# Kernel optimization log

Hardware: AMD Instinct MI355X
Metric: run time of the kernel (lower is better)

The kernel has to match this reference:

```python
import jax, jax.numpy as jnp
import numpy as np

F_NHID = 64
C_NHID = 64
U_INIT = F_NHID + C_NHID + 1   # 129
U_OUT = F_NHID + C_NHID        # 128
U_HID = 128
N_AGG = 4
M_INIT = 3 * N_AGG * U_OUT + C_NHID  # 1600
M_HID = 256
M_OUT = C_NHID


def setup_inputs() -> dict:
    key = jax.random.key(0)
    ks = jax.random.split(key, 12)
    B, Nc, Nf = 4, 512, 256
    h_fac = jax.random.normal(ks[0], (B, Nf, F_NHID), dtype=jnp.float32)
    h_cus = jax.random.normal(ks[1], (B, Nc, C_NHID), dtype=jnp.float32)
    edge = jax.random.normal(ks[2], (B, Nc, Nf, 1), dtype=jnp.float32)
    adj = jax.random.randint(ks[3], (B, Nc, Nf), 0, 2).astype(jnp.float32)
    def lin(k, i, o):
        return jax.random.normal(k, (i, o), dtype=jnp.float32) / np.sqrt(i)
    return {
        'h_fac': h_fac, 'h_cus': h_cus, 'edge': edge, 'adj': adj,
        'U_W1': lin(ks[4], U_INIT, U_HID), 'U_b1': jnp.zeros((U_HID,), jnp.float32),
        'U_W2': lin(ks[5], U_HID, U_OUT), 'U_b2': jnp.zeros((U_OUT,), jnp.float32),
        'M_W1': lin(ks[6], M_INIT, M_HID), 'M_b1': jnp.zeros((M_HID,), jnp.float32),
        'M_W2': lin(ks[7], M_HID, M_OUT), 'M_b2': jnp.zeros((M_OUT,), jnp.float32),
    }


def reference(h_fac, h_cus, edge, adj, U_W1, U_b1, U_W2, U_b2, M_W1, M_b1, M_W2, M_b2):
    B, Nc, c = h_cus.shape
    Nf = h_fac.shape[1]
    # Per-edge message input: [customer_feat, facility_feat, edge_scalar] -> (B,Nc,Nf,U_INIT)
    msg = jnp.concatenate([
        jnp.broadcast_to(h_cus[:, :, None, :], (B, Nc, Nf, c)),
        jnp.broadcast_to(h_fac[:, None, :, :], (B, Nc, Nf, h_fac.shape[-1])),
        edge,
    ], axis=-1)
    # U MLP (pretransformation): relu -> linear
    m = jax.nn.relu(msg @ U_W1 + U_b1)
    m = m @ U_W2 + U_b2  # (B, Nc, Nf, U_OUT)

    mask = adj > 0                              # (B, Nc, Nf)
    maskf = mask[..., None].astype(m.dtype)     # (B, Nc, Nf, 1)
    cnt = jnp.sum(maskf, axis=2)                # (B, Nc, 1)
    mean = jnp.sum(m * maskf, axis=2) / cnt     # nanmean over masked entries
    var = jnp.sum(((m - mean[:, :, None, :]) ** 2) * maskf, axis=2) / cnt
    std = jnp.sqrt(var)                         # population std (divides by count)
    mx = jnp.max(jnp.where(mask[..., None], m, -jnp.inf), axis=2)
    mn = jnp.min(jnp.where(mask[..., None], m, jnp.inf), axis=2)

    # Degree-based scalers (get_avgd + scale_amplification/attenuation)
    deg_c = jnp.sum(adj, axis=-1)               # (B, Nc)
    deg_f = jnp.sum(adj, axis=-2)               # (B, Nf)
    avg_d = jnp.mean(jnp.concatenate([jnp.log(deg_c + 1.0), jnp.log(deg_f + 1.0)], axis=-1), axis=-1)  # (B,)
    scale = (jnp.log(deg_c + 1.0) / avg_d[:, None])[..., None]          # (B, Nc, 1)
    scale_inv = jnp.where(scale != 0, 1.0 / scale, jnp.zeros_like(scale))

    feats = [h_cus]
    for a in (mean, std, mx, mn):
        feats.extend([a, a * scale, a * scale_inv])
    h = jnp.concatenate(feats, axis=-1)         # (B, Nc, M_INIT)

    # M MLP (posttransformation): relu -> linear (last activation 'none')
    h = jax.nn.relu(h @ M_W1 + M_b1)
    out = h @ M_W2 + M_b2                       # (B, Nc, C_NHID)
    return out
```

## Files before the change

kernel.cpp:

```cpp
#include <hip/hip_runtime.h>


using bs8 = __attribute__((ext_vector_type(8))) short;
using f4  = __attribute__((ext_vector_type(4))) float;

__device__ __forceinline__ unsigned short f2bf(float f) {
    union { float f; unsigned int u; } x; x.f = f;
    unsigned int u = x.u + 0x7FFFu + ((x.u >> 16) & 1u);
    return (unsigned short)(u >> 16);
}

__global__ void PNALayer_35081292874189_kernel() {}

#define OFF_AC     0u
#define OFF_AF     1048576u
#define OFF_DEGC   1572864u
#define OFF_DEGF   1581056u
#define OFF_SCALE  1585152u
#define OFF_SINV   1593344u
#define OFF_FEATB  1601536u
#define OFF_HMID   8155392u
#define OFF_W2T    10252544u
#define OFF_W1TB   10318080u
#define WS_NEED    11170048u

__global__ void PNALayer_ws_fail(float* out, int n) {
    int i = blockIdx.x * 256 + threadIdx.x;
    if (i < n) out[i] = 2500.0f;
}

__global__ void PNALayer_prep1(
    const float* h_fac, const float* h_cus, const float* adj,
    const float* U_W1, const float* U_b1, const float* U_W2, const float* M_W1,
    float* wsAc, float* wsAf, float* wsDegC, float* wsDegF,
    float* wsW2T, unsigned short* wsW1Tb)
{
    __shared__ float sH[64];
    __shared__ float sRed[256];
    __shared__ float sT[64][65];
    int bid = blockIdx.x, t = threadIdx.x;

    if (bid < 1024) {
        int b = bid >> 8, f = bid & 255;
        if (t < 64) sH[t] = h_fac[(b * 256 + f) * 64 + t];
        __syncthreads();
        if (t < 128) {
            float acc = 0.f;
            for (int k = 0; k < 64; ++k)
                acc += sH[k] * U_W1[(64 + k) * 128 + t];
            wsAf[(b * 256 + f) * 128 + t] = acc;
        }
        float v = adj[(b * 512 + t) * 256 + f] + adj[(b * 512 + t + 256) * 256 + f];
        sRed[t] = v; __syncthreads();
        for (int s = 128; s > 0; s >>= 1) { if (t < s) sRed[t] += sRed[t + s]; __syncthreads(); }
        if (t == 0) wsDegF[b * 256 + f] = sRed[0];
    } else if (bid < 3072) {
        int bc = bid - 1024;
        if (t < 64) sH[t] = h_cus[bc * 64 + t];
        __syncthreads();
        if (t < 128) {
            float acc = U_b1[t];
            for (int k = 0; k < 64; ++k)
                acc += sH[k] * U_W1[k * 128 + t];
            wsAc[bc * 128 + t] = acc;
        }
        float v = adj[bc * 256 + t];
        sRed[t] = v; __syncthreads();
        for (int s = 128; s > 0; s >>= 1) { if (t < s) sRed[t] += sRed[t + s]; __syncthreads(); }
        if (t == 0) wsDegC[bc] = sRed[0];
    } else if (bid < 3076) {
        int l = bid - 3072;
        int k0 = (l >> 1) * 64, n0 = (l & 1) * 64;
        for (int rep = 0; rep < 16; ++rep) {
            int idx = rep * 256 + t; int r = idx >> 6, c = idx & 63;
            sT[r][c] = U_W2[(k0 + r) * 128 + n0 + c];
        }
        __syncthreads();
        for (int rep = 0; rep < 16; ++rep) {
            int idx = rep * 256 + t; int r = idx >> 6, c = idx & 63;
            wsW2T[(n0 + r) * 128 + k0 + c] = sT[c][r];
        }
    } else if (bid < 3176) {
        int l = bid - 3076;
        int k0 = (l % 25) * 64, n0 = (l / 25) * 64;
        for (int rep = 0; rep < 16; ++rep) {
            int idx = rep * 256 + t; int r = idx >> 6, c = idx & 63;
            sT[r][c] = M_W1[(k0 + r) * 256 + n0 + c];
        }
        __syncthreads();
        for (int rep = 0; rep < 16; ++rep) {
            int idx = rep * 256 + t; int r = idx >> 6, c = idx & 63;
            wsW1Tb[(n0 + r) * 1664 + k0 + c] = f2bf(sT[c][r]);
        }
    } else {
        for (int i = 0; i < 64; ++i) {
            int idx = i * 256 + t;
            int n = idx >> 6, k = 1600 + (idx & 63);
            wsW1Tb[n * 1664 + k] = 0;
        }
    }
}

__global__ void PNALayer_prep2(
    const float* wsDegC, const float* wsDegF, float* wsScale, float* wsSinv)
{
    __shared__ float sRed[256];
    __shared__ float sAvg;
    int b = blockIdx.x, t = threadIdx.x;
    float v = logf(wsDegC[b * 512 + t] + 1.f) + logf(wsDegC[b * 512 + t + 256] + 1.f)
            + logf(wsDegF[b * 256 + t] + 1.f);
    sRed[t] = v; __syncthreads();
    for (int s = 128; s > 0; s >>= 1) { if (t < s) sRed[t] += sRed[t + s]; __syncthreads(); }
    if (t == 0) sAvg = sRed[0] / 768.f;
    __syncthreads();
    float avg = sAvg;
    for (int c = t; c < 512; c += 256) {
        float lg = logf(wsDegC[b * 512 + c] + 1.f);
        float sc = lg / avg;
        float si = (sc != 0.f) ? 1.f / sc : 0.f;
        wsScale[b * 512 + c] = sc;
        wsSinv[b * 512 + c] = si;
    }
}

__global__ __launch_bounds__(256, 2) void PNALayer_edge(
    const float* h_cus, const float* edge, const float* adj,
    const float* U_W1, const float* U_b2,
    const float* wsAc, const float* wsAf, const float* wsW2T, const float* wsDegC,
    const float* wsScale, const float* wsSinv,
    unsigned short* featB)
{
    __shared__ __align__(16) unsigned char smem[64000];
    unsigned short* sW2T = (unsigned short*)(smem);
    unsigned short* sM1  = (unsigned short*)(smem + 34816);
    float* sRed = (float*)(smem + 52224);
    float* sE   = (float*)(smem + 60416);
    float* sMk  = (float*)(smem + 61440);
    float* sAc  = (float*)(smem + 62464);
    float* sWe  = (float*)(smem + 62976);
    float* sB2  = (float*)(smem + 63488);

    int bc = blockIdx.x;
    int b  = bc >> 9;
    int t  = threadIdx.x;
    int w = t >> 6, quad = (t >> 4) & 3, ln = t & 15;

    {
        unsigned int* z = (unsigned int*)smem;
        for (int i = t; i < 16000; i += 256) z[i] = 0u;
    }
    __syncthreads();

    for (int rep = 0; rep < 16; ++rep) {
        int vi = rep * 256 + t;
        int n = vi >> 5, kb = (vi & 31) * 4;
        float4 wv = *(const float4*)(wsW2T + n * 128 + kb);
        uint2 p;
        p.x = (unsigned int)f2bf(wv.x) | ((unsigned int)f2bf(wv.y) << 16);
        p.y = (unsigned int)f2bf(wv.z) | ((unsigned int)f2bf(wv.w) << 16);
        *(uint2*)(sW2T + n * 136 + kb) = p;
    }
    sE[t]  = edge[bc * 256 + t];
    sMk[t] = (adj[bc * 256 + t] > 0.f) ? 1.f : 0.f;
    if (t < 128) {
        sAc[t] = wsAc[bc * 128 + t];
        sWe[t] = U_W1[128 * 128 + t];
        sB2[t] = U_b2[t];
    }
    __syncthreads();

    float b2v[8];
    for (int nt = 0; nt < 8; ++nt) b2v[nt] = sB2[nt * 16 + ln];

    float aS[8], aQ[8], aMx[8], aMn[8];
    for (int j = 0; j < 8; ++j) { aS[j] = 0.f; aQ[j] = 0.f; aMx[j] = -1e30f; aMn[j] = 1e30f; }

    for (int ft = 0; ft < 4; ++ft) {
        for (int i = 0; i < 8; ++i) {
            int idx = i * 256 + t;
            int fl = idx >> 5, k = (idx & 31) * 4;
            int f = ft * 64 + fl;
            float4 af = *(const float4*)(wsAf + (b * 256 + f) * 128 + k);
            float e = sE[f];
            float m0 = fmaxf(sAc[k + 0] + af.x + e * sWe[k + 0], 0.f);
            float m1 = fmaxf(sAc[k + 1] + af.y + e * sWe[k + 1], 0.f);
            float m2 = fmaxf(sAc[k + 2] + af.z + e * sWe[k + 2], 0.f);
            float m3 = fmaxf(sAc[k + 3] + af.w + e * sWe[k + 3], 0.f);
            uint2 p;
            p.x = (unsigned int)f2bf(m0) | ((unsigned int)f2bf(m1) << 16);
            p.y = (unsigned int)f2bf(m2) | ((unsigned int)f2bf(m3) << 16);
            *(uint2*)(sM1 + fl * 136 + k) = p;
        }
        __syncthreads();

        f4 acc[8];
        for (int nt = 0; nt < 8; ++nt) acc[nt] = (f4){0.f, 0.f, 0.f, 0.f};
        int arow = w * 16 + ln;
        for (int kk = 0; kk < 4; ++kk) {
            int ko = kk * 32 + quad * 8;
            bs8 a = *(const bs8*)(sM1 + arow * 136 + ko);
            for (int nt = 0; nt < 8; ++nt) {
                bs8 bb = *(const bs8*)(sW2T + (nt * 16 + ln) * 136 + ko);
                acc[nt] = __builtin_amdgcn_mfma_f32_16x16x32_bf16(a, bb, acc[nt], 0, 0, 0);
            }
        }

        for (int i = 0; i < 4; ++i) {
            int f = ft * 64 + w * 16 + quad * 4 + i;
            if (sMk[f] > 0.f) {
                for (int nt = 0; nt < 8; ++nt) {
                    float v = acc[nt][i] + b2v[nt];
                    aS[nt] += v; aQ[nt] += v * v;
                    aMx[nt] = fmaxf(aMx[nt], v); aMn[nt] = fminf(aMn[nt], v);
                }
            }
        }
        __syncthreads();
    }

    for (int nt = 0; nt < 8; ++nt) {
        aS[nt]  += __shfl_xor(aS[nt], 16, 64);  aS[nt]  += __shfl_xor(aS[nt], 32, 64);
        aQ[nt]  += __shfl_xor(aQ[nt], 16, 64);  aQ[nt]  += __shfl_xor(aQ[nt], 32, 64);
        aMx[nt] = fmaxf(aMx[nt], __shfl_xor(aMx[nt], 16, 64));
        aMx[nt] = fmaxf(aMx[nt], __shfl_xor(aMx[nt], 32, 64));
        aMn[nt] = fminf(aMn[nt], __shfl_xor(aMn[nt], 16, 64));
        aMn[nt] = fminf(aMn[nt], __shfl_xor(aMn[nt], 32, 64));
    }
    if (quad == 0) {
        for (int nt = 0; nt < 8; ++nt) {
            int col = nt * 16 + ln;
            sRed[(0 * 4 + w) * 128 + col] = aS[nt];
            sRed[(1 * 4 + w) * 128 + col] = aQ[nt];
            sRed[(2 * 4 + w) * 128 + col] = aMx[nt];
            sRed[(3 * 4 + w) * 128 + col] = aMn[nt];
        }
    }
    __syncthreads();

    if (t < 128) {
        int j = t;
        float rS = 0.f, rQ = 0.f, rMx = -1e30f, rMn = 1e30f;
        for (int ww = 0; ww < 4; ++ww) {
            rS += sRed[(0 * 4 + ww) * 128 + j];
            rQ += sRed[(1 * 4 + ww) * 128 + j];
            rMx = fmaxf(rMx, sRed[(2 * 4 + ww) * 128 + j]);
            rMn = fminf(rMn, sRed[(3 * 4 + ww) * 128 + j]);
        }
        float cnt = wsDegC[bc];
        float mean = rS / cnt;
        float var  = fmaxf(rQ / cnt - mean * mean, 0.f);
        float stdv = sqrtf(var);
        float sc = wsScale[bc], si = wsSinv[bc];
        unsigned short* fr = featB + bc * 1600;
        fr[64 + j]   = f2bf(mean); fr[192 + j]  = f2bf(mean * sc); fr[320 + j]  = f2bf(mean * si);
        fr[448 + j]  = f2bf(stdv); fr[576 + j]  = f2bf(stdv * sc); fr[704 + j]  = f2bf(stdv * si);
        fr[832 + j]  = f2bf(rMx);  fr[960 + j]  = f2bf(rMx * sc);  fr[1088 + j] = f2bf(rMx * si);
        fr[1216 + j] = f2bf(rMn);  fr[1344 + j] = f2bf(rMn * sc);  fr[1472 + j] = f2bf(rMn * si);
    } else if (t < 192) {
        int j = t - 128;
        featB[bc * 1600 + j] = f2bf(h_cus[bc * 64 + j]);
    }
}

__global__ __launch_bounds__(256) void PNALayer_mlp1(
    const unsigned short* featB, const unsigned short* wsW1Tb, const float* M_b1,
    float* h_mid)
{
    __shared__ __align__(16) unsigned short sA[16 * 136];
    __shared__ __align__(16) unsigned short sB[64 * 136];
    int t = threadIdx.x;
    int rb = (blockIdx.x >> 2) * 16, cb = (blockIdx.x & 3) * 64;
    int w = t >> 6, quad = (t >> 4) & 3, ln = t & 15;

    f4 acc = (f4){0.f, 0.f, 0.f, 0.f};

    for (int kt = 0; kt < 13; ++kt) {
        int kb = kt * 128;
        {
            int row = t >> 4, c8 = (t & 15) * 8;
            *(uint4*)(sA + row * 136 + c8) =
                *(const uint4*)(featB + (rb + row) * 1600 + kb + c8);
        }
        for (int i = 0; i < 4; ++i) {
            int vi = i * 256 + t;
            int row = vi >> 4, c8 = (vi & 15) * 8;
            *(uint4*)(sB + row * 136 + c8) =
                *(const uint4*)(wsW1Tb + (cb + row) * 1664 + kb + c8);
        }
        __syncthreads();
        for (int kk = 0; kk < 4; ++kk) {
            int ko = kk * 32 + quad * 8;
            bs8 a = *(const bs8*)(sA + ln * 136 + ko);
            bs8 bb = *(const bs8*)(sB + (w * 16 + ln) * 136 + ko);
            acc = __builtin_amdgcn_mfma_f32_16x16x32_bf16(a, bb, acc, 0, 0, 0);
        }
        __syncthreads();
    }
    int col = cb + w * 16 + ln;
    float b1v = M_b1[col];
    for (int i = 0; i < 4; ++i) {
        int row = rb + quad * 4 + i;
        h_mid[row * 256 + col] = fmaxf(acc[i] + b1v, 0.f);
    }
}

__global__ void PNALayer_mlp2(
    const float* h_mid, const float* M_W2, const float* M_b2, float* out)
{
    int idx = blockIdx.x * 256 + threadIdx.x;
    int row = idx >> 6, j = idx & 63;
    float acc = M_b2[j];
    const float* hr = h_mid + row * 256;
    for (int k = 0; k < 256; ++k)
        acc += hr[k] * M_W2[k * 64 + j];
    out[idx] = acc;
}

extern "C" void kernel_launch(void* const* d_in, const int* in_sizes, int n_in,
                              void* d_out, int out_size, void* d_ws, size_t ws_size,
                              hipStream_t stream) {
    const float* h_fac = (const float*)d_in[0];
    const float* h_cus = (const float*)d_in[1];
    const float* edge  = (const float*)d_in[2];
    const float* adj   = (const float*)d_in[3];
    const float* U_W1  = (const float*)d_in[4];
    const float* U_b1  = (const float*)d_in[5];
    const float* U_W2  = (const float*)d_in[6];
    const float* U_b2  = (const float*)d_in[7];
    const float* M_W1  = (const float*)d_in[8];
    const float* M_b1  = (const float*)d_in[9];
    const float* M_W2  = (const float*)d_in[10];
    const float* M_b2  = (const float*)d_in[11];
    (void)in_sizes; (void)n_in;

    float* outp = (float*)d_out;
    int nblk_out = (out_size + 255) / 256;

    if (ws_size < (size_t)WS_NEED) {
        PNALayer_ws_fail<<<nblk_out, 256, 0, stream>>>(outp, out_size);
        return;
    }

    char* ws = (char*)d_ws;
    float*          wsAc   = (float*)(ws + OFF_AC);
    float*          wsAf   = (float*)(ws + OFF_AF);
    float*          wsDegC = (float*)(ws + OFF_DEGC);
    float*          wsDegF = (float*)(ws + OFF_DEGF);
    float*          wsScal = (float*)(ws + OFF_SCALE);
    float*          wsSinv = (float*)(ws + OFF_SINV);
    unsigned short* wsFeatB= (unsigned short*)(ws + OFF_FEATB);
    float*          wsHmid = (float*)(ws + OFF_HMID);
    float*          wsW2T  = (float*)(ws + OFF_W2T);
    unsigned short* wsW1Tb = (unsigned short*)(ws + OFF_W1TB);

    PNALayer_prep1<<<3177, 256, 0, stream>>>(
        h_fac, h_cus, adj, U_W1, U_b1, U_W2, M_W1,
        wsAc, wsAf, wsDegC, wsDegF, wsW2T, wsW1Tb);
    PNALayer_prep2<<<4, 256, 0, stream>>>(wsDegC, wsDegF, wsScal, wsSinv);
    PNALayer_edge<<<2048, 256, 0, stream>>>(
        h_cus, edge, adj, U_W1, U_b2,
        wsAc, wsAf, wsW2T, wsDegC, wsScal, wsSinv, wsFeatB);
    PNALayer_mlp1<<<512, 256, 0, stream>>>(wsFeatB, wsW1Tb, M_b1, wsHmid);
    PNALayer_mlp2<<<512, 256, 0, stream>>>(wsHmid, M_W2, M_b2, outp);
}
```

Measured before the change: 180.0 us.

## Keep U_W2 bf16 fragments in registers and split edge MFMA by output columns

The prep kernel now writes the transposed U_W2 directly in bf16. The edge kernel loads each wave's slice of those weights into registers instead of staging the full matrix in shared memory. Each wave now owns 32 output columns across all 64 facility rows, so the cross-wave shared-memory reduction and its barrier go away and shared memory drops enough to allow 4 blocks per CU. It also vectorizes the sAc/sWe reads and uses the packed bf16 conversion intrinsic. The cost is that each wave reads all A rows from LDS and register pressure rises under the tighter launch bound.

```diff
diff --git a/kernel.cpp b/kernel.cpp
--- a/kernel.cpp
+++ b/kernel.cpp
@@ -1,4 +1,5 @@
 #include <hip/hip_runtime.h>
+#include <hip/hip_bf16.h>
 
 
 using bs8 = __attribute__((ext_vector_type(8))) short;
@@ -8,6 +9,12 @@
     union { float f; unsigned int u; } x; x.f = f;
     unsigned int u = x.u + 0x7FFFu + ((x.u >> 16) & 1u);
     return (unsigned short)(u >> 16);
+}
+
+__device__ __forceinline__ unsigned int pkbf(float a, float b) {
+    __hip_bfloat162 h = __float22bfloat162_rn(make_float2(a, b));
+    union { __hip_bfloat162 h; unsigned int u; } c; c.h = h;
+    return c.u;
 }
 
 __global__ void PNALayer_35081292874189_kernel() {}
@@ -33,7 +40,7 @@
     const float* h_fac, const float* h_cus, const float* adj,
     const float* U_W1, const float* U_b1, const float* U_W2, const float* M_W1,
     float* wsAc, float* wsAf, float* wsDegC, float* wsDegF,
-    float* wsW2T, unsigned short* wsW1Tb)
+    unsigned short* wsW2Tb, unsigned short* wsW1Tb)
 {
     __shared__ float sH[64];
     __shared__ float sRed[256];
@@ -78,7 +85,7 @@
         __syncthreads();
         for (int rep = 0; rep < 16; ++rep) {
             int idx = rep * 256 + t; int r = idx >> 6, c = idx & 63;
-            wsW2T[(n0 + r) * 128 + k0 + c] = sT[c][r];
+            wsW2Tb[(n0 + r) * 128 + k0 + c] = f2bf(sT[c][r]);
         }
     } else if (bid < 3176) {
         int l = bid - 3076;
@@ -123,102 +130,104 @@
     }
 }
 
-__global__ __launch_bounds__(256, 2) void PNALayer_edge(
+__global__ __launch_bounds__(256, 4) void PNALayer_edge(
     const float* h_cus, const float* edge, const float* adj,
     const float* U_W1, const float* U_b2,
-    const float* wsAc, const float* wsAf, const float* wsW2T, const float* wsDegC,
-    const float* wsScale, const float* wsSinv,
+    const float* wsAc, const float* wsAf, const unsigned short* wsW2Tb,
+    const float* wsDegC, const float* wsScale, const float* wsSinv,
     unsigned short* featB)
 {
-    __shared__ __align__(16) unsigned char smem[64000];
-    unsigned short* sW2T = (unsigned short*)(smem);
-    unsigned short* sM1  = (unsigned short*)(smem + 34816);
-    float* sRed = (float*)(smem + 52224);
-    float* sE   = (float*)(smem + 60416);
-    float* sMk  = (float*)(smem + 61440);
-    float* sAc  = (float*)(smem + 62464);
-    float* sWe  = (float*)(smem + 62976);
-    float* sB2  = (float*)(smem + 63488);
+    __shared__ __align__(16) unsigned short sM1[64 * 136];
+    __shared__ float sE[256];
+    __shared__ float sMk[256];
+    __shared__ float sAc[128];
+    __shared__ float sWe[128];
 
     int bc = blockIdx.x;
     int b  = bc >> 9;
     int t  = threadIdx.x;
     int w = t >> 6, quad = (t >> 4) & 3, ln = t & 15;
 
-    {
-        unsigned int* z = (unsigned int*)smem;
-        for (int i = t; i < 16000; i += 256) z[i] = 0u;
-    }
-    __syncthreads();
-
-    for (int rep = 0; rep < 16; ++rep) {
-        int vi = rep * 256 + t;
-        int n = vi >> 5, kb = (vi & 31) * 4;
-        float4 wv = *(const float4*)(wsW2T + n * 128 + kb);
-        uint2 p;
-        p.x = (unsigned int)f2bf(wv.x) | ((unsigned int)f2bf(wv.y) << 16);
-        p.y = (unsigned int)f2bf(wv.z) | ((unsigned int)f2bf(wv.w) << 16);
-        *(uint2*)(sW2T + n * 136 + kb) = p;
-    }
+    int r0 = (w * 2 + 0) * 16 + ln;
+    int r1 = (w * 2 + 1) * 16 + ln;
+    bs8 bw0[4], bw1[4];
+#pragma unroll
+    for (int kk = 0; kk < 4; ++kk) {
+        bw0[kk] = *(const bs8*)(wsW2Tb + r0 * 128 + kk * 32 + quad * 8);
+        bw1[kk] = *(const bs8*)(wsW2Tb + r1 * 128 + kk * 32 + quad * 8);
+    }
+    float b2v0 = U_b2[r0], b2v1 = U_b2[r1];
+
     sE[t]  = edge[bc * 256 + t];
     sMk[t] = (adj[bc * 256 + t] > 0.f) ? 1.f : 0.f;
     if (t < 128) {
         sAc[t] = wsAc[bc * 128 + t];
         sWe[t] = U_W1[128 * 128 + t];
-        sB2[t] = U_b2[t];
-    }
+    }
+    if (t < 64) featB[bc * 1600 + t] = f2bf(h_cus[bc * 64 + t]);
     __syncthreads();
 
-    float b2v[8];
-    for (int nt = 0; nt < 8; ++nt) b2v[nt] = sB2[nt * 16 + ln];
-
-    float aS[8], aQ[8], aMx[8], aMn[8];
-    for (int j = 0; j < 8; ++j) { aS[j] = 0.f; aQ[j] = 0.f; aMx[j] = -1e30f; aMn[j] = 1e30f; }
+    float aS[2]  = {0.f, 0.f},     aQ[2]  = {0.f, 0.f};
+    float aMx[2] = {-1e30f, -1e30f}, aMn[2] = {1e30f, 1e30f};
 
     for (int ft = 0; ft < 4; ++ft) {
+#pragma unroll
         for (int i = 0; i < 8; ++i) {
             int idx = i * 256 + t;
             int fl = idx >> 5, k = (idx & 31) * 4;
             int f = ft * 64 + fl;
-            float4 af = *(const float4*)(wsAf + (b * 256 + f) * 128 + k);
+            float4 af  = *(const float4*)(wsAf + (b * 256 + f) * 128 + k);
+            float4 ac4 = *(const float4*)(sAc + k);
+            float4 we4 = *(const float4*)(sWe + k);
             float e = sE[f];
-            float m0 = fmaxf(sAc[k + 0] + af.x + e * sWe[k + 0], 0.f);
-            float m1 = fmaxf(sAc[k + 1] + af.y + e * sWe[k + 1], 0.f);
-            float m2 = fmaxf(sAc[k + 2] + af.z + e * sWe[k + 2], 0.f);
-            float m3 = fmaxf(sAc[k + 3] + af.w + e * sWe[k + 3], 0.f);
+            float m0 = fmaxf(ac4.x + af.x + e * we4.x, 0.f);
+            float m1 = fmaxf(ac4.y + af.y + e * we4.y, 0.f);
+            float m2 = fmaxf(ac4.z + af.z + e * we4.z, 0.f);
+            float m3 = fmaxf(ac4.w + af.w + e * we4.w, 0.f);
             uint2 p;
-            p.x = (unsigned int)f2bf(m0) | ((unsigned int)f2bf(m1) << 16);
-            p.y = (unsigned int)f2bf(m2) | ((unsigned int)f2bf(m3) << 16);
+            p.x = pkbf(m0, m1);
+            p.y = pkbf(m2, m3);
             *(uint2*)(sM1 + fl * 136 + k) = p;
         }
         __syncthreads();
 
-        f4 acc[8];
-        for (int nt = 0; nt < 8; ++nt) acc[nt] = (f4){0.f, 0.f, 0.f, 0.f};
-        int arow = w * 16 + ln;
+        f4 acc[4][2];
+#pragma unroll
+        for (int rt = 0; rt < 4; ++rt) {
+            acc[rt][0] = (f4){0.f, 0.f, 0.f, 0.f};
+            acc[rt][1] = (f4){0.f, 0.f, 0.f, 0.f};
+        }
+#pragma unroll
         for (int kk = 0; kk < 4; ++kk) {
             int ko = kk * 32 + quad * 8;
-            bs8 a = *(const bs8*)(sM1 + arow * 136 + ko);
-            for (int nt = 0; nt < 8; ++nt) {
-                bs8 bb = *(const bs8*)(sW2T + (nt * 16 + ln) * 136 + ko);
-                acc[nt] = __builtin_amdgcn_mfma_f32_16x16x32_bf16(a, bb, acc[nt], 0, 0, 0);
+#pragma unroll
+            for (int rt = 0; rt < 4; ++rt) {
+                bs8 a = *(const bs8*)(sM1 + (rt * 16 + ln) * 136 + ko);
+                acc[rt][0] = __builtin_amdgcn_mfma_f32_16x16x32_bf16(a, bw0[kk], acc[rt][0], 0, 0, 0);
+                acc[rt][1] = __builtin_amdgcn_mfma_f32_16x16x32_bf16(a, bw1[kk], acc[rt][1], 0, 0, 0);
             }
         }
 
-        for (int i = 0; i < 4; ++i) {
-            int f = ft * 64 + w * 16 + quad * 4 + i;
-            if (sMk[f] > 0.f) {
-                for (int nt = 0; nt < 8; ++nt) {
-                    float v = acc[nt][i] + b2v[nt];
-                    aS[nt] += v; aQ[nt] += v * v;
-                    aMx[nt] = fmaxf(aMx[nt], v); aMn[nt] = fminf(aMn[nt], v);
+#pragma unroll
+        for (int rt = 0; rt < 4; ++rt) {
+#pragma unroll
+            for (int i = 0; i < 4; ++i) {
+                int f = ft * 64 + rt * 16 + quad * 4 + i;
+                if (sMk[f] > 0.f) {
+                    float v0 = acc[rt][0][i] + b2v0;
+                    float v1 = acc[rt][1][i] + b2v1;
+                    aS[0] += v0; aQ[0] += v0 * v0;
+                    aMx[0] = fmaxf(aMx[0], v0); aMn[0] = fminf(aMn[0], v0);
+                    aS[1] += v1; aQ[1] += v1 * v1;
+                    aMx[1] = fmaxf(aMx[1], v1); aMn[1] = fminf(aMn[1], v1);
                 }
             }
         }
         __syncthreads();
     }
 
-    for (int nt = 0; nt < 8; ++nt) {
+#pragma unroll
+    for (int nt = 0; nt < 2; ++nt) {
         aS[nt]  += __shfl_xor(aS[nt], 16, 64);  aS[nt]  += __shfl_xor(aS[nt], 32, 64);
         aQ[nt]  += __shfl_xor(aQ[nt], 16, 64);  aQ[nt]  += __shfl_xor(aQ[nt], 32, 64);
         aMx[nt] = fmaxf(aMx[nt], __shfl_xor(aMx[nt], 16, 64));
@@ -226,39 +235,23 @@
         aMn[nt] = fminf(aMn[nt], __shfl_xor(aMn[nt], 16, 64));
         aMn[nt] = fminf(aMn[nt], __shfl_xor(aMn[nt], 32, 64));
     }
+
     if (quad == 0) {
-        for (int nt = 0; nt < 8; ++nt) {
-            int col = nt * 16 + ln;
-            sRed[(0 * 4 + w) * 128 + col] = aS[nt];
-            sRed[(1 * 4 + w) * 128 + col] = aQ[nt];
-            sRed[(2 * 4 + w) * 128 + col] = aMx[nt];
-            sRed[(3 * 4 + w) * 128 + col] = aMn[nt];
-        }
-    }
-    __syncthreads();
-
-    if (t < 128) {
-        int j = t;
-        float rS = 0.f, rQ = 0.f, rMx = -1e30f, rMn = 1e30f;
-        for (int ww = 0; ww < 4; ++ww) {
-            rS += sRed[(0 * 4 + ww) * 128 + j];
-            rQ += sRed[(1 * 4 + ww) * 128 + j];
-            rMx = fmaxf(rMx, sRed[(2 * 4 + ww) * 128 + j]);
-            rMn = fminf(rMn, sRed[(3 * 4 + ww) * 128 + j]);
-        }
         float cnt = wsDegC[bc];
-        float mean = rS / cnt;
-        float var  = fmaxf(rQ / cnt - mean * mean, 0.f);
-        float stdv = sqrtf(var);
         float sc = wsScale[bc], si = wsSinv[bc];
         unsigned short* fr = featB + bc * 1600;
-        fr[64 + j]   = f2bf(mean); fr[192 + j]  = f2bf(mean * sc); fr[320 + j]  = f2bf(mean * si);
-        fr[448 + j]  = f2bf(stdv); fr[576 + j]  = f2bf(stdv * sc); fr[704 + j]  = f2bf(stdv * si);
-        fr[832 + j]  = f2bf(rMx);  fr[960 + j]  = f2bf(rMx * sc);  fr[1088 + j] = f2bf(rMx * si);
-        fr[1216 + j] = f2bf(rMn);  fr[1344 + j] = f2bf(rMn * sc);  fr[1472 + j] = f2bf(rMn * si);
-    } else if (t < 192) {
-        int j = t - 128;
-        featB[bc * 1600 + j] = f2bf(h_cus[bc * 64 + j]);
+#pragma unroll
+        for (int nt = 0; nt < 2; ++nt) {
+            int col = (w * 2 + nt) * 16 + ln;
+            float mean = aS[nt] / cnt;
+            float var  = fmaxf(aQ[nt] / cnt - mean * mean, 0.f);
+            float stdv = sqrtf(var);
+            float mx = aMx[nt], mn = aMn[nt];
+            fr[64 + col]   = f2bf(mean); fr[192 + col]  = f2bf(mean * sc); fr[320 + col]  = f2bf(mean * si);
+            fr[448 + col]  = f2bf(stdv); fr[576 + col]  = f2bf(stdv * sc); fr[704 + col]  = f2bf(stdv * si);
+            fr[832 + col]  = f2bf(mx);   fr[960 + col]  = f2bf(mx * sc);   fr[1088 + col] = f2bf(mx * si);
+            fr[1216 + col] = f2bf(mn);   fr[1344 + col] = f2bf(mn * sc);   fr[1472 + col] = f2bf(mn * si);
+        }
     }
 }
 
@@ -350,16 +343,16 @@
     float*          wsSinv = (float*)(ws + OFF_SINV);
     unsigned short* wsFeatB= (unsigned short*)(ws + OFF_FEATB);
     float*          wsHmid = (float*)(ws + OFF_HMID);
-    float*          wsW2T  = (float*)(ws + OFF_W2T);
+    unsigned short* wsW2Tb = (unsigned short*)(ws + OFF_W2T);
     unsigned short* wsW1Tb = (unsigned short*)(ws + OFF_W1TB);
 
     PNALayer_prep1<<<3177, 256, 0, stream>>>(
         h_fac, h_cus, adj, U_W1, U_b1, U_W2, M_W1,
-        wsAc, wsAf, wsDegC, wsDegF, wsW2T, wsW1Tb);
+        wsAc, wsAf, wsDegC, wsDegF, wsW2Tb, wsW1Tb);
     PNALayer_prep2<<<4, 256, 0, stream>>>(wsDegC, wsDegF, wsScal, wsSinv);
     PNALayer_edge<<<2048, 256, 0, stream>>>(
         h_cus, edge, adj, U_W1, U_b2,
-        wsAc, wsAf, wsW2T, wsDegC, wsScal, wsSinv, wsFeatB);
+        wsAc, wsAf, wsW2Tb, wsDegC, wsScal, wsSinv, wsFeatB);
     PNALayer_mlp1<<<512, 256, 0, stream>>>(wsFeatB, wsW1Tb, M_b1, wsHmid);
     PNALayer_mlp2<<<512, 256, 0, stream>>>(wsHmid, M_W2, M_b2, outp);
 }
```

After: 153.0 us. 15.0% less time.
